# Kernel tuning notes

Hardware: AMD Instinct MI355X
Metric: run time of the kernel (lower is better)

## Reference

```python
import jax, jax.numpy as jnp
import numpy as np

S, B, E, D, H, F, L = 1024, 8, 768, 8, 8, 2048, 4
D = 1024  # HIDDEN_DIM
H = 8     # nhead
DH = D // H
EPS = 1e-5


def _ln(x, g, b):
    m = jnp.mean(x, -1, keepdims=True)
    v = jnp.mean(jnp.square(x - m), -1, keepdims=True)
    return (x - m) * jax.lax.rsqrt(v + EPS) * g + b


def setup_inputs() -> dict:
    key = jax.random.key(0)
    ks = iter(jax.random.split(key, 16))
    n = lambda shape: jax.random.normal(next(ks), shape, jnp.float32) * 0.02
    return dict(
        x=jax.random.normal(next(ks), (S, B, E), jnp.float32),
        enc_w=n((D, E)), enc_b=jnp.zeros((D,), jnp.float32),
        enc_ln_g=jnp.ones((D,), jnp.float32), enc_ln_b=jnp.zeros((D,), jnp.float32),
        qkv_w=n((L, 3 * D, D)), qkv_b=jnp.zeros((L, 3 * D), jnp.float32),
        out_w=n((L, D, D)), out_b=jnp.zeros((L, D), jnp.float32),
        ln1_g=jnp.ones((L, D), jnp.float32), ln1_b=jnp.zeros((L, D), jnp.float32),
        ff1_w=n((L, F, D)), ff1_b=jnp.zeros((L, F), jnp.float32),
        ff2_w=n((L, D, F)), ff2_b=jnp.zeros((L, D), jnp.float32),
        ln2_g=jnp.ones((L, D), jnp.float32), ln2_b=jnp.zeros((L, D), jnp.float32),
        dec_w1=n((D // 2, D)), dec_b1=jnp.zeros((D // 2,), jnp.float32),
        dec_ln_g=jnp.ones((D // 2,), jnp.float32), dec_ln_b=jnp.zeros((D // 2,), jnp.float32),
        dec_w2=n((E, D // 2)), dec_b2=jnp.zeros((E,), jnp.float32),
    )


def reference(x, enc_w, enc_b, enc_ln_g, enc_ln_b, qkv_w, qkv_b, out_w, out_b,
              ln1_g, ln1_b, ff1_w, ff1_b, ff2_w, ff2_b, ln2_g, ln2_b,
              dec_w1, dec_b1, dec_ln_g, dec_ln_b, dec_w2, dec_b2):
    # encoder MLP: Linear -> LayerNorm -> ReLU (dropout = identity at eval)
    h = jax.nn.relu(_ln(x @ enc_w.T + enc_b, enc_ln_g, enc_ln_b))  # (S,B,D)
    scale = np.float32(1.0 / np.sqrt(DH))
    for l in range(L):  # 4 post-norm TransformerEncoderLayers, eager attention
        qkv = h @ qkv_w[l].T + qkv_b[l]                    # (S,B,3D)
        q, k, v = jnp.split(qkv, 3, axis=-1)
        q = q.reshape(S, B, H, DH)
        k = k.reshape(S, B, H, DH)
        v = v.reshape(S, B, H, DH)
        scores = jnp.einsum('sbhd,tbhd->bhst', q, k) * scale  # (B,H,S,S)
        p = jax.nn.softmax(scores, axis=-1)
        o = jnp.einsum('bhst,tbhd->sbhd', p, v).reshape(S, B, D)
        o = o @ out_w[l].T + out_b[l]
        h = _ln(h + o, ln1_g[l], ln1_b[l])
        f = jax.nn.relu(h @ ff1_w[l].T + ff1_b[l]) @ ff2_w[l].T + ff2_b[l]
        h = _ln(h + f, ln2_g[l], ln2_b[l])
    # decoder MLP
    d = jax.nn.relu(_ln(h @ dec_w1.T + dec_b1, dec_ln_g, dec_ln_b))
    return d @ dec_w2.T + dec_b2  # (S,B,E)
```

## Files before the change

kernel.cpp:

```cpp
#include <hip/hip_runtime.h>
#include <math.h>

#define S_ 1024
#define B_ 8
#define E_ 768
#define D_ 1024
#define H_ 8
#define F_ 2048
#define L_ 4
#define M_ (S_*B_)

typedef unsigned short u16;
typedef unsigned int u32;
typedef u16 u16x8 __attribute__((ext_vector_type(8)));
typedef u16 u16x4 __attribute__((ext_vector_type(4)));
typedef u16 u16x2 __attribute__((ext_vector_type(2)));
typedef u32 u32x2 __attribute__((ext_vector_type(2)));
typedef short bf16x8 __attribute__((ext_vector_type(8)));
typedef float f32x4 __attribute__((ext_vector_type(4)));

#define AS1 __attribute__((address_space(1)))
#define AS3 __attribute__((address_space(3)))

#define QSCALE 0.127517432f

__device__ __forceinline__ void gload_lds16(const void* g, void* l) {
  __builtin_amdgcn_global_load_lds((const AS1 void*)g, (AS3 void*)l, 16, 0, 0);
}
__device__ __forceinline__ u16 f2bf(float f) {
  unsigned u = __builtin_bit_cast(unsigned, f);
  return (u16)((u + 0x7fffu + ((u >> 16) & 1u)) >> 16);
}
__device__ __forceinline__ float bf2f(u16 h) {
  unsigned u = ((unsigned)h) << 16;
  return __builtin_bit_cast(float, u);
}
__device__ __forceinline__ u32 cvtpk(float a, float b) {
  u32 r;
  asm("v_cvt_pk_bf16_f32 %0, %1, %2" : "=v"(r) : "v"(a), "v"(b));
  return r;
}

__global__ __launch_bounds__(256) void conv4(
    const float* __restrict__ s0, u16* __restrict__ d0, int n0,
    const float* __restrict__ s1, u16* __restrict__ d1, int n1,
    const float* __restrict__ s2, u16* __restrict__ d2, int n2,
    const float* __restrict__ s3, u16* __restrict__ d3, int n3)
{
  int total = (n0 + n1 + n2 + n3) >> 2;
  for (int i = blockIdx.x * 256 + threadIdx.x; i < total; i += gridDim.x * 256) {
    int e = i << 2;
    const float* s; u16* d; int off;
    if (e < n0)           { s = s0; d = d0; off = e; }
    else if (e < n0+n1)   { s = s1; d = d1; off = e - n0; }
    else if (e < n0+n1+n2){ s = s2; d = d2; off = e - n0 - n1; }
    else                  { s = s3; d = d3; off = e - n0 - n1 - n2; }
    float4 v = *(const float4*)&s[off];
    u16x4 o; o[0]=f2bf(v.x); o[1]=f2bf(v.y); o[2]=f2bf(v.z); o[3]=f2bf(v.w);
    *(u16x4*)&d[off] = o;
  }
}

template<int ACT, int OUTBF, int SCQ, int RES>
__global__ __launch_bounds__(256) void gemm128(
    const u16* __restrict__ A, const u16* __restrict__ W,
    const float* __restrict__ bias, const u16* __restrict__ Rres,
    void* __restrict__ Cout, int M, int N, int K)
{
  __shared__ u16 lds[24576];
  const int gx = gridDim.x, nwg = gx * gridDim.y;
  const int lin = blockIdx.y * gx + blockIdx.x;
  const int work = (lin & 7) * (nwg >> 3) + (lin >> 3);
  const int bm = (work / gx) * 128, bn = (work % gx) * 128;
  const int tid = threadIdx.x;
  const int l = tid & 63;
  const int w = tid >> 6;
  const int l15 = l & 15, lg = l >> 4;
  const int wr = w >> 1, wc = w & 1;
  const int srow = tid >> 2;
  const int scb  = tid & 3;

  f32x4 acc[4][4] = {};
  const int nt = K >> 5;

#define STAGE(c, k0)                                                        \
  {                                                                         \
    u16* Ab = lds + (c)*8192;                                               \
    u16* Bb = Ab + 4096;                                                    \
    _Pragma("unroll")                                                       \
    for (int u = 0; u < 2; ++u) {                                           \
      int row = u*64 + srow;                                                \
      int cb  = scb ^ (row & 3);                                            \
      gload_lds16(A + (size_t)(bm + row) * K + (k0) + cb*8,                 \
                  Ab + u*2048 + tid*8);                                     \
      gload_lds16(W + (size_t)(bn + row) * K + (k0) + cb*8,                 \
                  Bb + u*2048 + tid*8);                                     \
    }                                                                       \
  }

  STAGE(0, 0);
  STAGE(1, 32);
  asm volatile("s_waitcnt vmcnt(4)" ::: "memory");
  __builtin_amdgcn_s_barrier();

  int cr = 0, cw = 2;
  for (int t = 0; t < nt; ++t) {
    if (t + 2 < nt) STAGE(cw, (t + 2) << 5);
    const u16* Ab = lds + cr*8192;
    const u16* Bb = Ab + 4096;
    bf16x8 af[4], bf_[4];
    #pragma unroll
    for (int mi = 0; mi < 4; ++mi) {
      int row = wr*64 + mi*16 + l15;
      af[mi] = *(const bf16x8*)&Ab[row*32 + (lg ^ (row & 3))*8];
    }
    #pragma unroll
    for (int ni = 0; ni < 4; ++ni) {
      int row = wc*64 + ni*16 + l15;
      bf_[ni] = *(const bf16x8*)&Bb[row*32 + (lg ^ (row & 3))*8];
    }
    #pragma unroll
    for (int mi = 0; mi < 4; ++mi)
      #pragma unroll
      for (int ni = 0; ni < 4; ++ni)
        acc[mi][ni] = __builtin_amdgcn_mfma_f32_16x16x32_bf16(af[mi], bf_[ni], acc[mi][ni], 0, 0, 0);
    if (t + 1 < nt) {
      if (t + 2 < nt) { asm volatile("s_waitcnt vmcnt(4)" ::: "memory"); }
      else            { asm volatile("s_waitcnt vmcnt(0)" ::: "memory"); }
      __builtin_amdgcn_s_barrier();
    }
    cr = (cr == 2) ? 0 : cr + 1;
    cw = (cw == 2) ? 0 : cw + 1;
  }
#undef STAGE

  u16* Cb = (u16*)Cout; float* Cf = (float*)Cout;
  #pragma unroll
  for (int ni = 0; ni < 4; ++ni) {
    int col = bn + wc*64 + ni*16 + l15;
    float bv = bias[col];
    #pragma unroll
    for (int mi = 0; mi < 4; ++mi) {
      #pragma unroll
      for (int rr = 0; rr < 4; ++rr) {
        int row = bm + wr*64 + mi*16 + lg*4 + rr;
        float v = acc[mi][ni][rr] + bv;
        if (RES) v += bf2f(Rres[(size_t)row * N + col]);
        if (ACT) v = fmaxf(v, 0.f);
        if (SCQ) { if (col < 1024) v *= QSCALE; }
        if (OUTBF) Cb[(size_t)row * N + col] = f2bf(v);
        else       Cf[(size_t)row * N + col] = v;
      }
    }
  }
}

template<int NV, bool RESID, bool RELU>
__global__ __launch_bounds__(256) void ln_bf16(
    const u16* __restrict__ X, const u16* __restrict__ R,
    const float* __restrict__ g, const float* __restrict__ b,
    u16* __restrict__ Y)
{
  constexpr int D = NV * 256;
  __shared__ float sbuf[8];
  const int tid = threadIdx.x;
  const size_t base = (size_t)blockIdx.x * D + tid * NV;
  float v[NV];
  if constexpr (NV == 4) {
    u16x4 xv = *(const u16x4*)&X[base];
    #pragma unroll
    for (int i = 0; i < 4; ++i) v[i] = bf2f(xv[i]);
    if (RESID) {
      u16x4 rv = *(const u16x4*)&R[base];
      #pragma unroll
      for (int i = 0; i < 4; ++i) v[i] += bf2f(rv[i]);
    }
  } else {
    u16x2 xv = *(const u16x2*)&X[base];
    #pragma unroll
    for (int i = 0; i < 2; ++i) v[i] = bf2f(xv[i]);
    if (RESID) {
      u16x2 rv = *(const u16x2*)&R[base];
      #pragma unroll
      for (int i = 0; i < 2; ++i) v[i] += bf2f(rv[i]);
    }
  }
  float sum = 0.f, sq = 0.f;
  #pragma unroll
  for (int i = 0; i < NV; ++i) { sum += v[i]; sq += v[i]*v[i]; }
  #pragma unroll
  for (int off = 32; off > 0; off >>= 1) {
    sum += __shfl_down(sum, off);
    sq  += __shfl_down(sq, off);
  }
  if ((tid & 63) == 0) { sbuf[tid >> 6] = sum; sbuf[4 + (tid >> 6)] = sq; }
  __syncthreads();
  sum = sbuf[0] + sbuf[1] + sbuf[2] + sbuf[3];
  sq  = sbuf[4] + sbuf[5] + sbuf[6] + sbuf[7];
  const float mean = sum / (float)D;
  const float rstd = rsqrtf(sq / (float)D - mean*mean + 1e-5f);
  const int c0 = tid * NV;
  if constexpr (NV == 4) {
    u16x4 o;
    #pragma unroll
    for (int i = 0; i < 4; ++i) {
      float t = (v[i] - mean) * rstd * g[c0+i] + b[c0+i];
      if (RELU) t = fmaxf(t, 0.f);
      o[i] = f2bf(t);
    }
    *(u16x4*)&Y[base] = o;
  } else {
    u16x2 o;
    #pragma unroll
    for (int i = 0; i < 2; ++i) {
      float t = (v[i] - mean) * rstd * g[c0+i] + b[c0+i];
      if (RELU) t = fmaxf(t, 0.f);
      o[i] = f2bf(t);
    }
    *(u16x2*)&Y[base] = o;
  }
}

__global__ __launch_bounds__(256) void vtrans(
    const u16* __restrict__ QKV, u16* __restrict__ Vt)
{
  __shared__ u16 Ls[32*132];
  const int st = blockIdx.x, bh = blockIdx.y;
  const int bb = bh >> 3, hh = bh & 7;
  const int t = threadIdx.x;
  #pragma unroll
  for (int i = 0; i < 2; ++i) {
    int e = i*256 + t;
    int s = e >> 4, d0 = (e & 15) * 8;
    u16x8 v = *(const u16x8*)&QKV[(size_t)((st*32 + s)*8 + bb)*3072 + 2048 + hh*128 + d0];
    #pragma unroll
    for (int j = 0; j < 4; ++j) {
      u16x2 p; p[0] = v[2*j]; p[1] = v[2*j+1];
      *(u16x2*)&Ls[s*132 + d0 + 2*j] = p;
    }
  }
  __syncthreads();
  #pragma unroll
  for (int i = 0; i < 2; ++i) {
    int e = i*256 + t;
    int d = e >> 2, s0 = (e & 3) * 8;
    u16x8 v;
    #pragma unroll
    for (int j = 0; j < 8; ++j) v[j] = Ls[(s0+j)*132 + d];
    *(u16x8*)&Vt[(size_t)bh*131072 + (size_t)d*1024 + st*32 + s0] = v;
  }
}

__global__ __launch_bounds__(512, 4) void attn_mfma(
    const u16* __restrict__ QKV, const u16* __restrict__ Vt,
    u16* __restrict__ AO)
{
  __shared__ u16 Ks[2][64*128];
  __shared__ u16 Vs[2][128*64];
  __shared__ u16 Pl[8][16*64];
  const int bid = blockIdx.x;
  const int wg = (bid & 7) * 64 + (bid >> 3);
  const int qt = wg & 7, bh = wg >> 3;
  const int bb = bh >> 3, hh = bh & 7;
  const int tid = threadIdx.x, w = tid >> 6, l = tid & 63;
  const int l15 = l & 15, lg = l >> 4;

  bf16x8 aq[4];
  {
    int q = qt*128 + w*16 + l15;
    const u16* qp = QKV + (size_t)(q*8 + bb)*3072 + hh*128 + lg*8;
    #pragma unroll
    for (int kc = 0; kc < 4; ++kc)
      aq[kc] = *(const bf16x8*)(qp + kc*32);
  }
  const u16* vbase = Vt + (size_t)bh*131072;

#define STAGE_KV(c, kt)                                                     \
  {                                                                         \
    _Pragma("unroll")                                                       \
    for (int i = 0; i < 2; ++i) {                                           \
      int e = (w*2 + i) * 512 + l * 8;                                      \
      int krow = e >> 7, d0 = e & 127;                                      \
      int dsw = d0 ^ ((krow & 7) << 3);                                     \
      gload_lds16(QKV + (size_t)(((kt)*64 + krow)*8 + bb)*3072 + 1024       \
                      + hh*128 + dsw,                                       \
                  &Ks[c][(w*2 + i) * 512]);                                 \
      int vd = e >> 6, vc = e & 63;                                         \
      int vsw = vc ^ ((vd & 7) << 3);                                       \
      gload_lds16(vbase + (size_t)vd*1024 + (kt)*64 + vsw,                  \
                  &Vs[c][(w*2 + i) * 512]);                                 \
    }                                                                       \
  }

  f32x4 of[8] = {};
  float mreg = -INFINITY, lpart = 0.f;
  const int psw = (l15 & 7) << 3;

  STAGE_KV(0, 0);
  __syncthreads();

  for (int kt = 0; kt < 16; ++kt) {
    const int cur = kt & 1;
    if (kt + 1 < 16) STAGE_KV(cur ^ 1, kt + 1);

    f32x4 sf[4] = {};
    #pragma unroll
    for (int kc = 0; kc < 4; ++kc) {
      #pragma unroll
      for (int f = 0; f < 4; ++f) {
        int krow = f*16 + l15;
        bf16x8 bk = *(const bf16x8*)&Ks[cur][krow*128 + ((kc*32 + lg*8) ^ ((krow & 7) << 3))];
        sf[f] = __builtin_amdgcn_mfma_f32_16x16x32_bf16(bk, aq[kc], sf[f], 0, 0, 0);
      }
    }

    float pm01 = fmaxf(fmaxf(sf[0][0], sf[0][1]), fmaxf(sf[0][2], sf[0][3]));
    float pm23 = fmaxf(fmaxf(sf[1][0], sf[1][1]), fmaxf(sf[1][2], sf[1][3]));
    float pm45 = fmaxf(fmaxf(sf[2][0], sf[2][1]), fmaxf(sf[2][2], sf[2][3]));
    float pm67 = fmaxf(fmaxf(sf[3][0], sf[3][1]), fmaxf(sf[3][2], sf[3][3]));
    float pmax = fmaxf(fmaxf(pm01, pm23), fmaxf(pm45, pm67));
    pmax = fmaxf(pmax, __shfl_xor(pmax, 16));
    pmax = fmaxf(pmax, __shfl_xor(pmax, 32));

    if (__any(pmax > mreg + 8.f)) {
      float mn = fmaxf(mreg, pmax);
      float al = exp2f(mreg - mn);
      mreg = mn;
      lpart *= al;
      #pragma unroll
      for (int r = 0; r < 4; ++r) {
        float alq = __shfl(al, (l & 48) + lg*4 + r);
        #pragma unroll
        for (int ni = 0; ni < 8; ++ni) of[ni][r] *= alq;
      }
    }

    float psum = 0.f;
    #pragma unroll
    for (int f = 0; f < 4; ++f) {
      float p0 = exp2f(sf[f][0] - mreg);
      float p1 = exp2f(sf[f][1] - mreg);
      float p2 = exp2f(sf[f][2] - mreg);
      float p3 = exp2f(sf[f][3] - mreg);
      psum += (p0 + p1) + (p2 + p3);
      u32x2 pk; pk[0] = cvtpk(p0, p1); pk[1] = cvtpk(p2, p3);
      *(u32x2*)&Pl[w][l15*64 + ((f*16 + lg*4) ^ psw)] = pk;
    }
    lpart += psum;

    bf16x8 pa0 = *(const bf16x8*)&Pl[w][l15*64 + ((lg*8) ^ psw)];
    bf16x8 pa1 = *(const bf16x8*)&Pl[w][l15*64 + ((32 + lg*8) ^ psw)];
    #pragma unroll
    for (int ni = 0; ni < 8; ++ni) {
      int n = ni*16 + l15;
      int nsw = (n & 7) << 3;
      bf16x8 vb0 = *(const bf16x8*)&Vs[cur][n*64 + ((lg*8) ^ nsw)];
      bf16x8 vb1 = *(const bf16x8*)&Vs[cur][n*64 + ((32 + lg*8) ^ nsw)];
      of[ni] = __builtin_amdgcn_mfma_f32_16x16x32_bf16(pa0, vb0, of[ni], 0, 0, 0);
      of[ni] = __builtin_amdgcn_mfma_f32_16x16x32_bf16(pa1, vb1, of[ni], 0, 0, 0);
    }

    if (kt + 1 < 16) __syncthreads();
  }
#undef STAGE_KV

  float ls = lpart;
  ls += __shfl_xor(ls, 16);
  ls += __shfl_xor(ls, 32);
  float inv = 1.f / ls;
  #pragma unroll
  for (int r = 0; r < 4; ++r) {
    float invq = __shfl(inv, (l & 48) + lg*4 + r);
    int q = qt*128 + w*16 + lg*4 + r;
    size_t base = (size_t)(q*8 + bb) * 1024 + hh*128;
    #pragma unroll
    for (int ni = 0; ni < 8; ++ni)
      AO[base + ni*16 + l15] = f2bf(of[ni][r] * invq);
  }
}

#define O_WENC  0ull
#define O_WDEC1 786432ull
#define O_WDEC2 1310720ull
#define O_WLQ   1703936ull
#define O_WLO   4849664ull
#define O_WLF1  5898240ull
#define O_WLF2  7995392ull
#define O_R     10092544ull
#define O_H     35258368ull
#define O_AO    43646976ull
#define O_VT    52035584ull

extern "C" void kernel_launch(void* const* d_in, const int* in_sizes, int n_in,
                              void* d_out, int out_size, void* d_ws, size_t ws_size,
                              hipStream_t stream) {
  (void)in_sizes; (void)n_in; (void)out_size; (void)ws_size;
  const float* x        = (const float*)d_in[0];
  const float* enc_w    = (const float*)d_in[1];
  const float* enc_b    = (const float*)d_in[2];
  const float* enc_ln_g = (const float*)d_in[3];
  const float* enc_ln_b = (const float*)d_in[4];
  const float* qkv_w    = (const float*)d_in[5];
  const float* qkv_b    = (const float*)d_in[6];
  const float* out_w    = (const float*)d_in[7];
  const float* out_b    = (const float*)d_in[8];
  const float* ln1_g    = (const float*)d_in[9];
  const float* ln1_b    = (const float*)d_in[10];
  const float* ff1_w    = (const float*)d_in[11];
  const float* ff1_b    = (const float*)d_in[12];
  const float* ff2_w    = (const float*)d_in[13];
  const float* ff2_b    = (const float*)d_in[14];
  const float* ln2_g    = (const float*)d_in[15];
  const float* ln2_b    = (const float*)d_in[16];
  const float* dec_w1   = (const float*)d_in[17];
  const float* dec_b1   = (const float*)d_in[18];
  const float* dec_ln_g = (const float*)d_in[19];
  const float* dec_ln_b = (const float*)d_in[20];
  const float* dec_w2   = (const float*)d_in[21];
  const float* dec_b2   = (const float*)d_in[22];

  u16* ws16 = (u16*)d_ws;
  u16* wenc  = ws16 + O_WENC;
  u16* wdec1 = ws16 + O_WDEC1;
  u16* wdec2 = ws16 + O_WDEC2;
  u16* wlq   = ws16 + O_WLQ;
  u16* wlo   = ws16 + O_WLO;
  u16* wlf1  = ws16 + O_WLF1;
  u16* wlf2  = ws16 + O_WLF2;
  u16* qkv   = ws16 + O_R;
  u16* bufY  = ws16 + O_R;
  u16* bufG  = ws16 + O_R + 8388608ull;
  u16* xb    = bufG;
  u16* dech  = bufG;
  u16* h     = ws16 + O_H;
  u16* ao    = ws16 + O_AO;
  u16* vt    = ws16 + O_VT;

  const dim3 blk(256);
  const dim3 blk5(512);

  conv4<<<1024, blk, 0, stream>>>(x, xb, 8192*768,
                                  enc_w, wenc, 1024*768,
                                  dec_w1, wdec1, 512*1024,
                                  dec_w2, wdec2, 768*512);
  gemm128<0,1,0,0><<<dim3(8,64), blk, 0, stream>>>(xb, wenc, enc_b, nullptr, bufY, M_, 1024, 768);
  ln_bf16<4,false,true><<<M_, blk, 0, stream>>>(bufY, nullptr, enc_ln_g, enc_ln_b, h);

  for (int l = 0; l < L_; ++l) {
    conv4<<<1024, blk, 0, stream>>>(qkv_w + (size_t)l*3145728, wlq, 3145728,
                                    out_w + (size_t)l*1048576, wlo, 1048576,
                                    ff1_w + (size_t)l*2097152, wlf1, 2097152,
                                    ff2_w + (size_t)l*2097152, wlf2, 2097152);
    gemm128<0,1,1,0><<<dim3(24,64), blk, 0, stream>>>(h, wlq, qkv_b + (size_t)l*3072, nullptr, qkv, M_, 3072, 1024);
    vtrans<<<dim3(32,64), blk, 0, stream>>>(qkv, vt);
    attn_mfma<<<512, blk5, 0, stream>>>(qkv, vt, ao);
    gemm128<0,1,0,1><<<dim3(8,64), blk, 0, stream>>>(ao, wlo, out_b + (size_t)l*1024, h, bufY, M_, 1024, 1024);
    ln_bf16<4,false,false><<<M_, blk, 0, stream>>>(bufY, nullptr, ln1_g + (size_t)l*1024, ln1_b + (size_t)l*1024, h);
    gemm128<1,1,0,0><<<dim3(16,64), blk, 0, stream>>>(h, wlf1, ff1_b + (size_t)l*2048, nullptr, bufG, M_, 2048, 1024);
    gemm128<0,1,0,1><<<dim3(8,64), blk, 0, stream>>>(bufG, wlf2, ff2_b + (size_t)l*1024, h, bufY, M_, 1024, 2048);
    ln_bf16<4,false,false><<<M_, blk, 0, stream>>>(bufY, nullptr, ln2_g + (size_t)l*1024, ln2_b + (size_t)l*1024, h);
  }

  gemm128<0,1,0,0><<<dim3(4,64), blk, 0, stream>>>(h, wdec1, dec_b1, nullptr, bufY, M_, 512, 1024);
  ln_bf16<2,false,true><<<M_, blk, 0, stream>>>(bufY, nullptr, dec_ln_g, dec_ln_b, dech);
  gemm128<0,0,0,0><<<dim3(6,64), blk, 0, stream>>>(dech, wdec2, dec_b2, nullptr, d_out, M_, 768, 512);
}
```

Before: 1.139 ms.

## Enlarge GEMM tiles to 256x128 with 512 threads and K-step 64

Replaces the 128x128 GEMM kernel (256 threads, K-step 32) with a 256x128 tile kernel using 8 waves, a K-step of 64, and an 8-way XOR swizzle in LDS. Each wave now computes a 128x32 sub-tile, and all GEMM launches halve their M grid dimension. The larger tile and deeper K chunk are meant to improve data reuse and cut barrier and load-issue overhead per FLOP. The cost is about 144KB of LDS for triple buffering, which limits occupancy to one block per CU, and fewer workgroups, which may hurt the smaller GEMMs. It also removes the unused residual path from the LayerNorm kernel.

Result: faster. 1.082 ms (-5.0%).

```diff
diff --git a/kernel.cpp b/kernel.cpp
--- a/kernel.cpp
+++ b/kernel.cpp
@@ -62,70 +62,78 @@
 }
 
 template<int ACT, int OUTBF, int SCQ, int RES>
-__global__ __launch_bounds__(256) void gemm128(
+__global__ __launch_bounds__(512) void gemm256(
     const u16* __restrict__ A, const u16* __restrict__ W,
     const float* __restrict__ bias, const u16* __restrict__ Rres,
     void* __restrict__ Cout, int M, int N, int K)
 {
-  __shared__ u16 lds[24576];
+  __shared__ u16 lds[73728];
   const int gx = gridDim.x, nwg = gx * gridDim.y;
   const int lin = blockIdx.y * gx + blockIdx.x;
   const int work = (lin & 7) * (nwg >> 3) + (lin >> 3);
-  const int bm = (work / gx) * 128, bn = (work % gx) * 128;
+  const int bm = (work / gx) * 256, bn = (work % gx) * 128;
   const int tid = threadIdx.x;
   const int l = tid & 63;
   const int w = tid >> 6;
   const int l15 = l & 15, lg = l >> 4;
-  const int wr = w >> 1, wc = w & 1;
-  const int srow = tid >> 2;
-  const int scb  = tid & 3;
-
-  f32x4 acc[4][4] = {};
-  const int nt = K >> 5;
+  const int wr = w >> 2, wc = w & 3;
+  const int srow = tid >> 3;
+  const int scb  = tid & 7;
+
+  f32x4 acc[8][2] = {};
+  const int nt = K >> 6;
 
 #define STAGE(c, k0)                                                        \
   {                                                                         \
-    u16* Ab = lds + (c)*8192;                                               \
-    u16* Bb = Ab + 4096;                                                    \
+    u16* Ab = lds + (c)*24576;                                              \
+    u16* Bb = Ab + 16384;                                                   \
+    _Pragma("unroll")                                                       \
+    for (int u = 0; u < 4; ++u) {                                           \
+      int row = u*64 + srow;                                                \
+      int cb  = scb ^ (row & 7);                                            \
+      gload_lds16(A + (size_t)(bm + row) * K + (k0) + cb*8,                 \
+                  Ab + u*4096 + tid*8);                                     \
+    }                                                                       \
     _Pragma("unroll")                                                       \
     for (int u = 0; u < 2; ++u) {                                           \
       int row = u*64 + srow;                                                \
-      int cb  = scb ^ (row & 3);                                            \
-      gload_lds16(A + (size_t)(bm + row) * K + (k0) + cb*8,                 \
-                  Ab + u*2048 + tid*8);                                     \
+      int cb  = scb ^ (row & 7);                                            \
       gload_lds16(W + (size_t)(bn + row) * K + (k0) + cb*8,                 \
-                  Bb + u*2048 + tid*8);                                     \
+                  Bb + u*4096 + tid*8);                                     \
     }                                                                       \
   }
 
   STAGE(0, 0);
-  STAGE(1, 32);
-  asm volatile("s_waitcnt vmcnt(4)" ::: "memory");
+  STAGE(1, 64);
+  asm volatile("s_waitcnt vmcnt(6)" ::: "memory");
   __builtin_amdgcn_s_barrier();
 
   int cr = 0, cw = 2;
   for (int t = 0; t < nt; ++t) {
-    if (t + 2 < nt) STAGE(cw, (t + 2) << 5);
-    const u16* Ab = lds + cr*8192;
-    const u16* Bb = Ab + 4096;
-    bf16x8 af[4], bf_[4];
-    #pragma unroll
-    for (int mi = 0; mi < 4; ++mi) {
-      int row = wr*64 + mi*16 + l15;
-      af[mi] = *(const bf16x8*)&Ab[row*32 + (lg ^ (row & 3))*8];
-    }
-    #pragma unroll
-    for (int ni = 0; ni < 4; ++ni) {
-      int row = wc*64 + ni*16 + l15;
-      bf_[ni] = *(const bf16x8*)&Bb[row*32 + (lg ^ (row & 3))*8];
-    }
-    #pragma unroll
-    for (int mi = 0; mi < 4; ++mi)
-      #pragma unroll
-      for (int ni = 0; ni < 4; ++ni)
-        acc[mi][ni] = __builtin_amdgcn_mfma_f32_16x16x32_bf16(af[mi], bf_[ni], acc[mi][ni], 0, 0, 0);
+    if (t + 2 < nt) STAGE(cw, (t + 2) << 6);
+    const u16* Ab = lds + cr*24576;
+    const u16* Bb = Ab + 16384;
+    #pragma unroll
+    for (int ks = 0; ks < 2; ++ks) {
+      bf16x8 af[8], bf_[2];
+      #pragma unroll
+      for (int mi = 0; mi < 8; ++mi) {
+        int row = wr*128 + mi*16 + l15;
+        af[mi] = *(const bf16x8*)&Ab[row*64 + ((ks*4 + lg) ^ (row & 7))*8];
+      }
+      #pragma unroll
+      for (int ni = 0; ni < 2; ++ni) {
+        int row = wc*32 + ni*16 + l15;
+        bf_[ni] = *(const bf16x8*)&Bb[row*64 + ((ks*4 + lg) ^ (row & 7))*8];
+      }
+      #pragma unroll
+      for (int mi = 0; mi < 8; ++mi)
+        #pragma unroll
+        for (int ni = 0; ni < 2; ++ni)
+          acc[mi][ni] = __builtin_amdgcn_mfma_f32_16x16x32_bf16(af[mi], bf_[ni], acc[mi][ni], 0, 0, 0);
+    }
     if (t + 1 < nt) {
-      if (t + 2 < nt) { asm volatile("s_waitcnt vmcnt(4)" ::: "memory"); }
+      if (t + 2 < nt) { asm volatile("s_waitcnt vmcnt(6)" ::: "memory"); }
       else            { asm volatile("s_waitcnt vmcnt(0)" ::: "memory"); }
       __builtin_amdgcn_s_barrier();
     }
@@ -136,14 +144,14 @@
 
   u16* Cb = (u16*)Cout; float* Cf = (float*)Cout;
   #pragma unroll
-  for (int ni = 0; ni < 4; ++ni) {
-    int col = bn + wc*64 + ni*16 + l15;
+  for (int ni = 0; ni < 2; ++ni) {
+    int col = bn + wc*32 + ni*16 + l15;
     float bv = bias[col];
     #pragma unroll
-    for (int mi = 0; mi < 4; ++mi) {
+    for (int mi = 0; mi < 8; ++mi) {
       #pragma unroll
       for (int rr = 0; rr < 4; ++rr) {
-        int row = bm + wr*64 + mi*16 + lg*4 + rr;
+        int row = bm + wr*128 + mi*16 + lg*4 + rr;
         float v = acc[mi][ni][rr] + bv;
         if (RES) v += bf2f(Rres[(size_t)row * N + col]);
         if (ACT) v = fmaxf(v, 0.f);
@@ -155,9 +163,9 @@
   }
 }
 
-template<int NV, bool RESID, bool RELU>
+template<int NV, bool RELU>
 __global__ __launch_bounds__(256) void ln_bf16(
-    const u16* __restrict__ X, const u16* __restrict__ R,
+    const u16* __restrict__ X,
     const float* __restrict__ g, const float* __restrict__ b,
     u16* __restrict__ Y)
 {
@@ -170,20 +178,10 @@
     u16x4 xv = *(const u16x4*)&X[base];
     #pragma unroll
     for (int i = 0; i < 4; ++i) v[i] = bf2f(xv[i]);
-    if (RESID) {
-      u16x4 rv = *(const u16x4*)&R[base];
-      #pragma unroll
-      for (int i = 0; i < 4; ++i) v[i] += bf2f(rv[i]);
-    }
   } else {
     u16x2 xv = *(const u16x2*)&X[base];
     #pragma unroll
     for (int i = 0; i < 2; ++i) v[i] = bf2f(xv[i]);
-    if (RESID) {
-      u16x2 rv = *(const u16x2*)&R[base];
-      #pragma unroll
-      for (int i = 0; i < 2; ++i) v[i] += bf2f(rv[i]);
-    }
   }
   float sum = 0.f, sq = 0.f;
   #pragma unroll
@@ -443,25 +441,25 @@
                                   enc_w, wenc, 1024*768,
                                   dec_w1, wdec1, 512*1024,
                                   dec_w2, wdec2, 768*512);
-  gemm128<0,1,0,0><<<dim3(8,64), blk, 0, stream>>>(xb, wenc, enc_b, nullptr, bufY, M_, 1024, 768);
-  ln_bf16<4,false,true><<<M_, blk, 0, stream>>>(bufY, nullptr, enc_ln_g, enc_ln_b, h);
+  gemm256<0,1,0,0><<<dim3(8,32), blk5, 0, stream>>>(xb, wenc, enc_b, nullptr, bufY, M_, 1024, 768);
+  ln_bf16<4,true><<<M_, blk, 0, stream>>>(bufY, enc_ln_g, enc_ln_b, h);
 
   for (int l = 0; l < L_; ++l) {
     conv4<<<1024, blk, 0, stream>>>(qkv_w + (size_t)l*3145728, wlq, 3145728,
                                     out_w + (size_t)l*1048576, wlo, 1048576,
                                     ff1_w + (size_t)l*2097152, wlf1, 2097152,
                                     ff2_w + (size_t)l*2097152, wlf2, 2097152);
-    gemm128<0,1,1,0><<<dim3(24,64), blk, 0, stream>>>(h, wlq, qkv_b + (size_t)l*3072, nullptr, qkv, M_, 3072, 1024);
+    gemm256<0,1,1,0><<<dim3(24,32), blk5, 0, stream>>>(h, wlq, qkv_b + (size_t)l*3072, nullptr, qkv, M_, 3072, 1024);
     vtrans<<<dim3(32,64), blk, 0, stream>>>(qkv, vt);
     attn_mfma<<<512, blk5, 0, stream>>>(qkv, vt, ao);
-    gemm128<0,1,0,1><<<dim3(8,64), blk, 0, stream>>>(ao, wlo, out_b + (size_t)l*1024, h, bufY, M_, 1024, 1024);
-    ln_bf16<4,false,false><<<M_, blk, 0, stream>>>(bufY, nullptr, ln1_g + (size_t)l*1024, ln1_b + (size_t)l*1024, h);
-    gemm128<1,1,0,0><<<dim3(16,64), blk, 0, stream>>>(h, wlf1, ff1_b + (size_t)l*2048, nullptr, bufG, M_, 2048, 1024);
-    gemm128<0,1,0,1><<<dim3(8,64), blk, 0, stream>>>(bufG, wlf2, ff2_b + (size_t)l*1024, h, bufY, M_, 1024, 2048);
-    ln_bf16<4,false,false><<<M_, blk, 0, stream>>>(bufY, nullptr, ln2_g + (size_t)l*1024, ln2_b + (size_t)l*1024, h);
-  }
-
-  gemm128<0,1,0,0><<<dim3(4,64), blk, 0, stream>>>(h, wdec1, dec_b1, nullptr, bufY, M_, 512, 1024);
-  ln_bf16<2,false,true><<<M_, blk, 0, stream>>>(bufY, nullptr, dec_ln_g, dec_ln_b, dech);
-  gemm128<0,0,0,0><<<dim3(6,64), blk, 0, stream>>>(dech, wdec2, dec_b2, nullptr, d_out, M_, 768, 512);
-}
+    gemm256<0,1,0,1><<<dim3(8,32), blk5, 0, stream>>>(ao, wlo, out_b + (size_t)l*1024, h, bufY, M_, 1024, 1024);
+    ln_bf16<4,false><<<M_, blk, 0, stream>>>(bufY, ln1_g + (size_t)l*1024, ln1_b + (size_t)l*1024, h);
+    gemm256<1,1,0,0><<<dim3(16,32), blk5, 0, stream>>>(h, wlf1, ff1_b + (size_t)l*2048, nullptr, bufG, M_, 2048, 1024);
+    gemm256<0,1,0,1><<<dim3(8,32), blk5, 0, stream>>>(bufG, wlf2, ff2_b + (size_t)l*1024, h, bufY, M_, 1024, 2048);
+    ln_bf16<4,false><<<M_, blk, 0, stream>>>(bufY, ln2_g + (size_t)l*1024, ln2_b + (size_t)l*1024, h);
+  }
+
+  gemm256<0,1,0,0><<<dim3(4,32), blk5, 0, stream>>>(h, wdec1, dec_b1, nullptr, bufY, M_, 512, 1024);
+  ln_bf16<2,true><<<M_, blk, 0, stream>>>(bufY, dec_ln_g, dec_ln_b, dech);
+  gemm256<0,0,0,0><<<dim3(6,32), blk5, 0, stream>>>(dech, wdec2, dec_b2, nullptr, d_out, M_, 768, 512);
+}
```
